# Kernel tuning notes

Hardware: AMD Instinct MI355X
Metric: run time of the kernel (lower is better)

Reference implementation:

```python
import jax, jax.numpy as jnp
import numpy as np

B, T, C = 2, 2048, 2048
N_HEAD, N_GROUPS, HEAD_SIZE = 16, 4, 128
Q_PER_KV = N_HEAD // N_GROUPS  # 4
N_ELEM = HEAD_SIZE  # rotary_percentage = 1.0
HIDDEN = 4 * C
EPS = 1e-5


def layernorm(x, w, b):
    m = jnp.mean(x, axis=-1, keepdims=True)
    v = jnp.mean(jnp.square(x - m), axis=-1, keepdims=True)
    return (x - m) * jax.lax.rsqrt(v + EPS) * w + b


def apply_rope(x, cos, sin):
    # x: [B, H, T, n_elem]; cos/sin: [T, n_elem] (broadcast over B, H)
    d = x.shape[-1]
    x1, x2 = x[..., : d // 2], x[..., d // 2 :]
    rotated = jnp.concatenate((-x2, x1), axis=-1)
    return x * cos + rotated * sin


def setup_inputs() -> dict:
    key = jax.random.key(0)
    ks = jax.random.split(key, 8)
    x = jax.random.normal(ks[0], (B, T, C), dtype=jnp.float32)
    # rope cache (NeoX/LLaMA half-rotation layout), base 10000
    theta = 1.0 / (10000.0 ** (jnp.arange(0, N_ELEM, 2, dtype=jnp.float32) / N_ELEM))
    idx_theta = jnp.outer(jnp.arange(T, dtype=jnp.float32), theta)  # [T, n_elem//2]
    idx_theta = jnp.concatenate((idx_theta, idx_theta), axis=-1)    # [T, n_elem]
    cos, sin = jnp.cos(idx_theta), jnp.sin(idx_theta)
    mask = jnp.tril(jnp.ones((T, T), dtype=bool))[None, None]  # causal [1,1,T,T]
    s = 0.02
    return {
        "x": x,
        "cos": cos,
        "sin": sin,
        "ln1_w": jnp.ones((C,), jnp.float32),
        "ln1_b": jnp.zeros((C,), jnp.float32),
        "ln2_w": jnp.ones((C,), jnp.float32),
        "ln2_b": jnp.zeros((C,), jnp.float32),
        "w_attn": jax.random.normal(ks[1], (C, (N_HEAD + 2 * N_GROUPS) * HEAD_SIZE), jnp.float32) * s,
        "w_proj": jax.random.normal(ks[2], (C, C), jnp.float32) * s,
        "w_fc": jax.random.normal(ks[3], (C, HIDDEN), jnp.float32) * s,
        "w_mlp_proj": jax.random.normal(ks[4], (HIDDEN, C), jnp.float32) * s,
        "mask": mask,
    }


def reference(x, cos, sin, ln1_w, ln1_b, ln2_w, ln2_b, w_attn, w_proj, w_fc, w_mlp_proj, mask):
    n1 = layernorm(x, ln1_w, ln1_b)
    # fused QKV projection
    qkv = n1 @ w_attn  # [B, T, (H + 2G) * hs]
    qkv = qkv.reshape(B, T, N_GROUPS, Q_PER_KV + 2, HEAD_SIZE)
    q = qkv[:, :, :, :Q_PER_KV]      # [B, T, G, qpk, hs]
    k = qkv[:, :, :, Q_PER_KV]       # [B, T, G, hs]
    v = qkv[:, :, :, Q_PER_KV + 1]   # [B, T, G, hs]
    # q -> [B, H, T, hs] (group-major head order)
    q = q.transpose(0, 2, 3, 1, 4).reshape(B, N_HEAD, T, HEAD_SIZE)
    # k, v -> [B, G, T, hs] then repeat_interleave groups to H heads
    k = jnp.repeat(k.transpose(0, 2, 1, 3), Q_PER_KV, axis=1)  # [B, H, T, hs]
    v = jnp.repeat(v.transpose(0, 2, 1, 3), Q_PER_KV, axis=1)
    # RoPE on the first N_ELEM dims (here full head)
    q = jnp.concatenate((apply_rope(q[..., :N_ELEM], cos, sin), q[..., N_ELEM:]), axis=-1)
    k = jnp.concatenate((apply_rope(k[..., :N_ELEM], cos, sin), k[..., N_ELEM:]), axis=-1)
    scale = 1.0 / np.sqrt(HEAD_SIZE).astype(np.float32)
    att = jnp.einsum("bhtd,bhsd->bhts", q, k) * scale
    att = jnp.where(mask, att, jnp.finfo(att.dtype).min)
    att = jax.nn.softmax(att, axis=-1)
    y = jnp.einsum("bhts,bhsd->bhtd", att, v)
    y = y.transpose(0, 2, 1, 3).reshape(B, T, C)
    h = y @ w_proj
    # non-parallel residual (LLaMA-style): x + attn, then x + mlp(norm2(x))
    x = x + h
    n2 = layernorm(x, ln2_w, ln2_b)
    mlp = jax.nn.gelu(n2 @ w_fc, approximate=False) @ w_mlp_proj
    return x + mlp
```

## Files before the change

### kernel.cpp

```cpp
#include <hip/hip_runtime.h>
#include <stdint.h>
#include <math.h>

#define Tn   2048
#define Cn   2048
#define BTn  4096
#define NQKV 3072
#define HID  8192

typedef unsigned short u16;
typedef float f32x4 __attribute__((ext_vector_type(4)));
typedef short s16x8 __attribute__((ext_vector_type(8)));

__device__ __forceinline__ float b2f(u16 u) { return __uint_as_float(((unsigned)u) << 16); }
__device__ __forceinline__ u16 f2b(float f) {
  unsigned i = __float_as_uint(f);
  return (u16)((i + 0x7fffu + ((i >> 16) & 1u)) >> 16);
}

__device__ __forceinline__ void g2l16(const void* g, void* l) {
  __builtin_amdgcn_global_load_lds((const __attribute__((address_space(1))) unsigned int*)g,
                                   (__attribute__((address_space(3))) unsigned int*)l,
                                   16, 0, 0);
}

__global__ __launch_bounds__(256) void transpose_f2b(const float* __restrict__ in,
                                                     u16* __restrict__ out, int R, int C) {
  __shared__ float tile[32][33];
  int bx = blockIdx.x * 32, by = blockIdx.y * 32;
  int tx = threadIdx.x, ty = threadIdx.y;
  #pragma unroll
  for (int j = 0; j < 32; j += 8)
    tile[ty + j][tx] = in[(size_t)(by + ty + j) * C + bx + tx];
  __syncthreads();
  #pragma unroll
  for (int j = 0; j < 32; j += 8)
    out[(size_t)(bx + ty + j) * R + by + tx] = f2b(tile[tx][ty + j]);
}

__global__ __launch_bounds__(256) void transpose_u16(const u16* __restrict__ in,
                                                     u16* __restrict__ out, int R, int C) {
  __shared__ u16 tile[32][33];
  const size_t zb = (size_t)blockIdx.z * R * C;
  int bx = blockIdx.x * 32, by = blockIdx.y * 32;
  int tx = threadIdx.x, ty = threadIdx.y;
  #pragma unroll
  for (int j = 0; j < 32; j += 8)
    tile[ty + j][tx] = in[zb + (size_t)(by + ty + j) * C + bx + tx];
  __syncthreads();
  #pragma unroll
  for (int j = 0; j < 32; j += 8)
    out[zb + (size_t)(bx + ty + j) * R + by + tx] = tile[tx][ty + j];
}

__global__ __launch_bounds__(256)
void copy_f32(const float* __restrict__ in, float* __restrict__ out) {
  const long i = ((long)blockIdx.x * 256 + threadIdx.x) * 4;
  *(f32x4*)(out + i) = *(const f32x4*)(in + i);
}

__global__ __launch_bounds__(256)
void layernorm_k(const float* __restrict__ x, const float* __restrict__ w,
                 const float* __restrict__ bb, u16* __restrict__ out) {
  __shared__ float red[256];
  __shared__ float sm, sv;
  const int tid = threadIdx.x;
  const long row = blockIdx.x;
  const float* xr = x + row * (long)Cn;
  float v[8];
  float s = 0.f;
  #pragma unroll
  for (int i = 0; i < 8; ++i) { v[i] = xr[i * 256 + tid]; s += v[i]; }
  red[tid] = s; __syncthreads();
  for (int st = 128; st > 0; st >>= 1) { if (tid < st) red[tid] += red[tid + st]; __syncthreads(); }
  if (tid == 0) sm = red[0] * (1.f / Cn);
  __syncthreads();
  const float mean = sm;
  float s2 = 0.f;
  #pragma unroll
  for (int i = 0; i < 8; ++i) { float d = v[i] - mean; s2 += d * d; }
  red[tid] = s2; __syncthreads();
  for (int st = 128; st > 0; st >>= 1) { if (tid < st) red[tid] += red[tid + st]; __syncthreads(); }
  if (tid == 0) sv = rsqrtf(red[0] * (1.f / Cn) + 1e-5f);
  __syncthreads();
  const float rstd = sv;
  #pragma unroll
  for (int i = 0; i < 8; ++i) {
    int c = i * 256 + tid;
    out[row * (long)Cn + c] = f2b((v[i] - mean) * rstd * w[c] + bb[c]);
  }
}

__global__ __launch_bounds__(256)
void rope_split(const u16* __restrict__ qkv, const float* __restrict__ cs,
                const float* __restrict__ sn, u16* __restrict__ q,
                u16* __restrict__ k, u16* __restrict__ v) {
  const long idx = (long)blockIdx.x * 256 + threadIdx.x;
  const int row = (int)(idx / NQKV);
  const int col = (int)(idx % NQKV);
  const int b = row >> 11, t = row & 2047;
  const int g = col / 768, rr = col % 768, s = rr >> 7, d = rr & 127;
  const u16 raw = qkv[idx];
  if (s == 5) { v[((long)(b * 4 + g) * Tn + t) * 128 + d] = raw; return; }
  const float xv = b2f(raw);
  const float x2 = b2f(qkv[idx - d + (d ^ 64)]);
  const float c = cs[t * 128 + d];
  const float si = sn[t * 128 + d];
  const float rot = (d < 64) ? -x2 : x2;
  const float o = xv * c + rot * si;
  if (s == 4) k[((long)(b * 4 + g) * Tn + t) * 128 + d] = f2b(o);
  else        q[((long)(b * 16 + g * 4 + s) * Tn + t) * 128 + d] = f2b(o);
}

__global__ __launch_bounds__(256, 2)
void attn_flash(const u16* __restrict__ q, const u16* __restrict__ k,
                const u16* __restrict__ vt, u16* __restrict__ y) {
  __shared__ __align__(16) u16 Ks[2 * 8192];
  __shared__ __align__(16) u16 Vs[2 * 8192];
  __shared__ __align__(16) u16 Ps[4][2 * 16 * 32];
  const int tid = threadIdx.x, wave = tid >> 6, lane = tid & 63;
  const int fr = lane & 15, quad = lane >> 4;
  const int lr4 = lane >> 2;
  const int su  = ((lr4 >> 3) & 1) << 1;
  const int lcs = (((lane & 3) ^ su) << 3);
  const int ksw = ((fr >> 3) & 1) << 1;
  const int rslot = (quad ^ ksw) << 3;
  const int bx = blockIdx.x, bh = blockIdx.y;
  const int b = bh >> 4, h = bh & 15, g = h >> 2;
  const int bg = b * 4 + g;
  const u16* kg = k + (size_t)bg * Tn * 128;
  const u16* vg = vt + (size_t)bg * 128 * Tn;
  const int q0 = bx * 64 + wave * 16;

  s16x8 qf[4];
  {
    const u16* qrow = q + ((size_t)bh * Tn + q0 + fr) * 128;
    #pragma unroll
    for (int kc = 0; kc < 4; ++kc)
      qf[kc] = *(const s16x8*)(qrow + kc * 32 + quad * 8);
  }
  f32x4 o_acc[8] = {};
  float m_r[4], l_r[4];
  #pragma unroll
  for (int r = 0; r < 4; ++r) { m_r[r] = -1e30f; l_r[r] = 0.f; }
  const float scale = 0.08838834764831845f;

  auto stage_kv = [&](int j0, int bufsel) {
    u16* kd = Ks + bufsel * 8192;
    u16* vd = Vs + bufsel * 8192;
    #pragma unroll
    for (int kc = 0; kc < 4; ++kc)
      g2l16(kg + (size_t)(j0 + wave * 16 + lr4) * 128 + kc * 32 + lcs,
            kd + kc * 2048 + wave * 512);
    #pragma unroll
    for (int kc = 0; kc < 2; ++kc)
      #pragma unroll
      for (int hh = 0; hh < 2; ++hh)
        g2l16(vg + (size_t)(wave * 32 + hh * 16 + lr4) * Tn + j0 + kc * 32 + lcs,
              vd + kc * 4096 + (wave * 32 + hh * 16) * 32);
  };

  stage_kv(0, 0);
  asm volatile("s_waitcnt vmcnt(0)" ::: "memory");
  __builtin_amdgcn_s_barrier();

  int cur = 0;
  for (int step = 0; step <= bx; ++step) {
    const int j0 = step * 64;
    if (step < bx) stage_kv(j0 + 64, cur ^ 1);
    const u16* kcur = Ks + cur * 8192;
    const u16* vcur = Vs + cur * 8192;

    f32x4 s[4] = {};
    __builtin_amdgcn_s_setprio(1);
    #pragma unroll
    for (int kc = 0; kc < 4; ++kc)
      #pragma unroll
      for (int nt = 0; nt < 4; ++nt) {
        s16x8 bf = *(const s16x8*)(kcur + kc * 2048 + (nt * 16 + fr) * 32 + rslot);
        s[nt] = __builtin_amdgcn_mfma_f32_16x16x32_bf16(qf[kc], bf, s[nt], 0, 0, 0);
      }
    __builtin_amdgcn_s_setprio(0);

    const bool diag = (step == bx);
    #pragma unroll
    for (int r = 0; r < 4; ++r) {
      float vmax = -1e30f;
      #pragma unroll
      for (int nt = 0; nt < 4; ++nt) {
        float sv = s[nt][r] * scale;
        if (diag && (j0 + nt * 16 + fr) > (q0 + quad * 4 + r)) sv = -1e30f;
        s[nt][r] = sv;
        vmax = fmaxf(vmax, sv);
      }
      #pragma unroll
      for (int mk = 1; mk < 16; mk <<= 1) vmax = fmaxf(vmax, __shfl_xor(vmax, mk, 64));
      const float mnew = fmaxf(m_r[r], vmax);
      const float alpha = __expf(m_r[r] - mnew);
      float rsum = 0.f;
      #pragma unroll
      for (int nt = 0; nt < 4; ++nt) {
        float pv = __expf(s[nt][r] - mnew);
        s[nt][r] = pv; rsum += pv;
      }
      #pragma unroll
      for (int mk = 1; mk < 16; mk <<= 1) rsum += __shfl_xor(rsum, mk, 64);
      l_r[r] = l_r[r] * alpha + rsum;
      m_r[r] = mnew;
      #pragma unroll
      for (int nt = 0; nt < 8; ++nt) o_acc[nt][r] *= alpha;
    }

    u16* pw = Ps[wave];
    #pragma unroll
    for (int nt = 0; nt < 4; ++nt) {
      const int col = nt * 16 + fr, pan = col >> 5, cc = col & 31;
      #pragma unroll
      for (int r = 0; r < 4; ++r) {
        const int prow = quad * 4 + r;
        pw[pan * 512 + prow * 32 + (cc ^ (((prow >> 3) & 1) << 4))] = f2b(s[nt][r]);
      }
    }
    #pragma unroll
    for (int kc = 0; kc < 2; ++kc) {
      s16x8 af = *(const s16x8*)(pw + kc * 512 + fr * 32 + rslot);
      __builtin_amdgcn_s_setprio(1);
      #pragma unroll
      for (int nt = 0; nt < 8; ++nt) {
        s16x8 bf = *(const s16x8*)(vcur + kc * 4096 + (nt * 16 + fr) * 32 + rslot);
        o_acc[nt] = __builtin_amdgcn_mfma_f32_16x16x32_bf16(af, bf, o_acc[nt], 0, 0, 0);
      }
      __builtin_amdgcn_s_setprio(0);
    }

    asm volatile("s_waitcnt vmcnt(0) lgkmcnt(0)" ::: "memory");
    __builtin_amdgcn_s_barrier();
    cur ^= 1;
  }

  #pragma unroll
  for (int r = 0; r < 4; ++r) {
    const float inv = 1.f / l_r[r];
    const size_t row = (size_t)(b * Tn + q0 + quad * 4 + r) * Cn + h * 128;
    #pragma unroll
    for (int nt = 0; nt < 8; ++nt)
      y[row + nt * 16 + fr] = f2b(o_acc[nt][r] * inv);
  }
}

#define BAR  __builtin_amdgcn_s_barrier()
#define LG0  asm volatile("s_waitcnt lgkmcnt(0)" ::: "memory")
#define RD_A(BUF, MI4)                                                                  \
  { _Pragma("unroll") for (int m_ = 0; m_ < 4; ++m_) {                                  \
      _Pragma("unroll") for (int k_ = 0; k_ < 2; ++k_)                                  \
        ar[m_][k_] = *(const s16x8*)(Sb + (BUF) * 32768 + aBase +                       \
                                     (((MI4) + m_) << 11) + (k_ << 10) + fragoff); } }
#define RD_B(BUF, NI2, DST)                                                             \
  { _Pragma("unroll") for (int n_ = 0; n_ < 2; ++n_) {                                  \
      _Pragma("unroll") for (int k_ = 0; k_ < 2; ++k_)                                  \
        DST[n_][k_] = *(const s16x8*)(Sb + (BUF) * 32768 + bBase +                      \
                                      (((NI2) + n_) << 11) + (k_ << 10) + fragoff); } }
#define MM(MB, NB, BR)                                                                  \
  { __builtin_amdgcn_s_setprio(1);                                                     \
    _Pragma("unroll") for (int m_ = 0; m_ < 4; ++m_) {                                  \
      _Pragma("unroll") for (int n_ = 0; n_ < 2; ++n_) {                                \
        _Pragma("unroll") for (int k_ = 0; k_ < 2; ++k_)                                \
          acc[(MB) + m_][(NB) + n_] = __builtin_amdgcn_mfma_f32_16x16x32_bf16(          \
              ar[m_][k_], BR[n_][k_], acc[(MB) + m_][(NB) + n_], 0, 0, 0); } }          \
    __builtin_amdgcn_s_setprio(0); }

template <int EPI>
__global__ __launch_bounds__(512, 2)
void gemm256(const u16* __restrict__ A, const u16* __restrict__ Bt,
             const float* __restrict__ res, u16* __restrict__ ob,
             float* __restrict__ of, int N, int Kl, int ld, int num_n) {
  __shared__ __align__(16) u16 S[65536];
  char* Sb = (char*)S;

  const long koff = (long)blockIdx.y * Kl;
  A += koff; Bt += koff;

  const int pid = blockIdx.x;
  const int xcd = pid & 7, idx = pid >> 3;
  const int jj = idx & 3;
  const int gp = (idx >> 2) * 8 + xcd;
  const int npc = num_n >> 1;
  const int pr = gp / npc, pc = gp - pr * npc;
  const long m0 = (long)(pr * 2 + (jj >> 1)) * 256;
  const long n0 = (long)(pc * 2 + (jj & 1)) * 256;

  const int tid = (int)threadIdx.x;
  const int wave = tid >> 6, lane = tid & 63;
  const int wr = wave >> 2, wc = wave & 3;
  const int fr = lane & 15, quad = lane >> 4;
  const int fragoff = (fr * 64 + quad * 16) ^ (((fr >> 3) & 1) << 5);
  const int aBase = wr * 16384;
  const int bBase = 65536 + (wc >> 1) * 16384 + ((wc & 1) << 13);

  int srow[2], skcb[2];
  #pragma unroll
  for (int rr = 0; rr < 2; ++rr) {
    const int d = rr * 8192 + wave * 1024 + lane * 16;
    const int l = d ^ (((d >> 9) & 1) << 5);
    srow[rr] = ((l >> 11) << 4) | ((l >> 6) & 15);
    skcb[rr] = (((l >> 10) & 1) << 6) | (l & 63);
  }
  auto stage = [&](const u16* __restrict__ src, long grow0, int kt, int regionByte) {
    #pragma unroll
    for (int rr = 0; rr < 2; ++rr)
      g2l16((const char*)src + (grow0 + srow[rr]) * (long)ld * 2 + (long)kt * 128 + skcb[rr],
            Sb + regionByte + rr * 8192 + wave * 1024);
  };

  const int nk = Kl >> 6;
  const int nk2 = nk >> 1;

  stage(A,  m0,       0, 0);
  stage(A,  m0 + 128, 0, 16384);
  stage(Bt, n0,       0, 65536);
  stage(Bt, n0 + 128, 0, 81920);
  stage(Bt, n0,       1, 98304);
  stage(Bt, n0 + 128, 1, 114688);
  asm volatile("s_waitcnt vmcnt(4)" ::: "memory");
  BAR;

  s16x8 ar[4][2], br0[2][2], br1[2][2];
  f32x4 acc[8][4] = {};

  for (int i = 0; i < nk2; ++i) {
    const int t1 = 2 * i + 1, s0 = 2 * i + 2, s1 = 2 * i + 3;
    const bool v0 = (s0 < nk), v1 = (s1 < nk);
    RD_A(0, 0); RD_B(0, 0, br0);
    stage(A, m0, t1, 32768);
    MM(0, 0, br0); LG0; BAR;
    RD_B(0, 2, br1);
    stage(A, m0 + 128, t1, 49152);
    MM(0, 2, br1); LG0; BAR;
    RD_A(0, 4);
    if (v0) stage(Bt, n0, s0, 65536);
    MM(4, 2, br1); LG0; BAR;
    if (v0) stage(Bt, n0 + 128, s0, 81920);
    MM(4, 0, br0);
    if (v0) { asm volatile("s_waitcnt vmcnt(4)" ::: "memory"); }
    else    { asm volatile("s_waitcnt vmcnt(0)" ::: "memory"); }
    BAR;
    RD_A(1, 0); RD_B(1, 0, br0);
    if (v0) stage(A, m0, s0, 0);
    MM(0, 0, br0); LG0; BAR;
    RD_B(1, 2, br1);
    if (v0) stage(A, m0 + 128, s0, 16384);
    MM(0, 2, br1); LG0; BAR;
    RD_A(1, 4);
    if (v1) stage(Bt, n0, s1, 98304);
    MM(4, 2, br1); LG0; BAR;
    if (v1) stage(Bt, n0 + 128, s1, 114688);
    MM(4, 0, br0);
    asm volatile("s_waitcnt vmcnt(4)" ::: "memory");
    BAR;
  }

  #pragma unroll
  for (int mi = 0; mi < 8; ++mi)
    #pragma unroll
    for (int ni = 0; ni < 4; ++ni)
      #pragma unroll
      for (int r = 0; r < 4; ++r) {
        const long row = m0 + wr * 128 + mi * 16 + quad * 4 + r;
        const long col = n0 + wc * 64 + ni * 16 + fr;
        const long idx2 = row * N + col;
        const float vv = acc[mi][ni][r];
        if (EPI == 0) ob[idx2] = f2b(vv);
        else if (EPI == 1) of[idx2] = vv + res[idx2];
        else if (EPI == 2) ob[idx2] = f2b(0.5f * vv * (1.0f + erff(vv * 0.70710678118654752f)));
        else atomicAdd(&of[idx2], vv);
      }
}

extern "C" void kernel_launch(void* const* d_in, const int* in_sizes, int n_in,
                              void* d_out, int out_size, void* d_ws, size_t ws_size,
                              hipStream_t stream) {
  (void)in_sizes; (void)n_in; (void)out_size; (void)ws_size;
  const float* x      = (const float*)d_in[0];
  const float* cosb   = (const float*)d_in[1];
  const float* sinb   = (const float*)d_in[2];
  const float* ln1w   = (const float*)d_in[3];
  const float* ln1b   = (const float*)d_in[4];
  const float* ln2w   = (const float*)d_in[5];
  const float* ln2b   = (const float*)d_in[6];
  const float* w_attn = (const float*)d_in[7];
  const float* w_proj = (const float*)d_in[8];
  const float* w_fc   = (const float*)d_in[9];
  const float* w_mp   = (const float*)d_in[10];
  float* out = (float*)d_out;

  char* p = (char*)d_ws;
  auto alloc = [&](size_t bytes) { char* r = p; p += (bytes + 255) & ~(size_t)255; return (void*)r; };
  u16*  wT_attn = (u16*)alloc((size_t)NQKV * Cn * 2);
  u16*  wT_proj = (u16*)alloc((size_t)Cn * Cn * 2);
  u16*  wT_fc   = (u16*)alloc((size_t)HID * Cn * 2);
  u16*  wT_mp   = (u16*)alloc((size_t)Cn * HID * 2);
  u16*  n12     = (u16*)alloc((size_t)BTn * Cn * 2);
  u16*  qkv     = (u16*)alloc((size_t)BTn * NQKV * 2);
  u16*  qb      = (u16*)alloc((size_t)2 * 16 * Tn * 128 * 2);
  u16*  kb      = (u16*)alloc((size_t)2 * 4 * Tn * 128 * 2);
  u16*  vb      = (u16*)alloc((size_t)2 * 4 * Tn * 128 * 2);
  float* x1     = (float*)alloc((size_t)BTn * Cn * 4);
  u16*  hbuf    = (u16*)alloc((size_t)BTn * HID * 2);
  u16*  vt      = n12;

  dim3 tb(32, 8);
  transpose_f2b<<<dim3(NQKV / 32, Cn / 32), tb, 0, stream>>>(w_attn, wT_attn, Cn, NQKV);
  transpose_f2b<<<dim3(Cn / 32, Cn / 32), tb, 0, stream>>>(w_proj, wT_proj, Cn, Cn);
  transpose_f2b<<<dim3(HID / 32, Cn / 32), tb, 0, stream>>>(w_fc, wT_fc, Cn, HID);
  transpose_f2b<<<dim3(Cn / 32, HID / 32), tb, 0, stream>>>(w_mp, wT_mp, HID, Cn);

  layernorm_k<<<BTn, 256, 0, stream>>>(x, ln1w, ln1b, n12);
  gemm256<0><<<(BTn / 256) * (NQKV / 256), 512, 0, stream>>>(n12, wT_attn, nullptr, qkv, nullptr, NQKV, Cn, Cn, NQKV / 256);
  rope_split<<<(int)(((long)BTn * NQKV) / 256), 256, 0, stream>>>(qkv, cosb, sinb, qb, kb, vb);
  transpose_u16<<<dim3(128 / 32, Tn / 32, 8), tb, 0, stream>>>(vb, vt, Tn, 128);
  attn_flash<<<dim3(Tn / 64, 32), 256, 0, stream>>>(qb, kb, vt, qkv );
  copy_f32<<<(int)(((long)BTn * Cn) / 1024), 256, 0, stream>>>(x, x1);
  gemm256<3><<<dim3((BTn / 256) * (Cn / 256), 2), 512, 0, stream>>>(qkv, wT_proj, nullptr, nullptr, x1, Cn, Cn / 2, Cn, Cn / 256);
  layernorm_k<<<BTn, 256, 0, stream>>>(x1, ln2w, ln2b, n12);
  gemm256<2><<<(BTn / 256) * (HID / 256), 512, 0, stream>>>(n12, wT_fc, nullptr, hbuf, nullptr, HID, Cn, Cn, HID / 256);
  copy_f32<<<(int)(((long)BTn * Cn) / 1024), 256, 0, stream>>>(x1, out);
  gemm256<3><<<dim3((BTn / 256) * (Cn / 256), 2), 512, 0, stream>>>(hbuf, wT_mp, nullptr, nullptr, out, Cn, HID / 2, HID, Cn / 256);
}
```

Measured before the change: 897.3 us.

## Replace staggered quarter-tile GEMM pipeline with simple double-buffered per-k-tile loop

Replaces the hand-scheduled ping-pong GEMM main loop with a plain double-buffered loop. The old loop split each k-tile into four MFMA phases with interleaved LDS reads, async global-to-LDS stages and barriers. The new loop loads all B fragments, issues the next tile's loads, runs the full 8x4 MFMA block while streaming A fragments, then waits on everything and hits one barrier per tile. This cuts barrier count and scheduling complexity, but it loses the fine-grained overlap, and the full vmcnt(0) wait exposes load latency at every tile.

Result: no change. 900.2 us (+0.3%).

```diff
diff --git a/kernel.cpp b/kernel.cpp
--- a/kernel.cpp
+++ b/kernel.cpp
@@ -249,25 +249,6 @@
 }
 
 #define BAR  __builtin_amdgcn_s_barrier()
-#define LG0  asm volatile("s_waitcnt lgkmcnt(0)" ::: "memory")
-#define RD_A(BUF, MI4)                                                                  \
-  { _Pragma("unroll") for (int m_ = 0; m_ < 4; ++m_) {                                  \
-      _Pragma("unroll") for (int k_ = 0; k_ < 2; ++k_)                                  \
-        ar[m_][k_] = *(const s16x8*)(Sb + (BUF) * 32768 + aBase +                       \
-                                     (((MI4) + m_) << 11) + (k_ << 10) + fragoff); } }
-#define RD_B(BUF, NI2, DST)                                                             \
-  { _Pragma("unroll") for (int n_ = 0; n_ < 2; ++n_) {                                  \
-      _Pragma("unroll") for (int k_ = 0; k_ < 2; ++k_)                                  \
-        DST[n_][k_] = *(const s16x8*)(Sb + (BUF) * 32768 + bBase +                      \
-                                      (((NI2) + n_) << 11) + (k_ << 10) + fragoff); } }
-#define MM(MB, NB, BR)                                                                  \
-  { __builtin_amdgcn_s_setprio(1);                                                     \
-    _Pragma("unroll") for (int m_ = 0; m_ < 4; ++m_) {                                  \
-      _Pragma("unroll") for (int n_ = 0; n_ < 2; ++n_) {                                \
-        _Pragma("unroll") for (int k_ = 0; k_ < 2; ++k_)                                \
-          acc[(MB) + m_][(NB) + n_] = __builtin_amdgcn_mfma_f32_16x16x32_bf16(          \
-              ar[m_][k_], BR[n_][k_], acc[(MB) + m_][(NB) + n_], 0, 0, 0); } }          \
-    __builtin_amdgcn_s_setprio(0); }
 
 template <int EPI>
 __global__ __launch_bounds__(512, 2)
@@ -313,49 +294,50 @@
   };
 
   const int nk = Kl >> 6;
-  const int nk2 = nk >> 1;
 
   stage(A,  m0,       0, 0);
   stage(A,  m0 + 128, 0, 16384);
   stage(Bt, n0,       0, 65536);
   stage(Bt, n0 + 128, 0, 81920);
-  stage(Bt, n0,       1, 98304);
-  stage(Bt, n0 + 128, 1, 114688);
-  asm volatile("s_waitcnt vmcnt(4)" ::: "memory");
+  asm volatile("s_waitcnt vmcnt(0)" ::: "memory");
   BAR;
 
-  s16x8 ar[4][2], br0[2][2], br1[2][2];
   f32x4 acc[8][4] = {};
 
-  for (int i = 0; i < nk2; ++i) {
-    const int t1 = 2 * i + 1, s0 = 2 * i + 2, s1 = 2 * i + 3;
-    const bool v0 = (s0 < nk), v1 = (s1 < nk);
-    RD_A(0, 0); RD_B(0, 0, br0);
-    stage(A, m0, t1, 32768);
-    MM(0, 0, br0); LG0; BAR;
-    RD_B(0, 2, br1);
-    stage(A, m0 + 128, t1, 49152);
-    MM(0, 2, br1); LG0; BAR;
-    RD_A(0, 4);
-    if (v0) stage(Bt, n0, s0, 65536);
-    MM(4, 2, br1); LG0; BAR;
-    if (v0) stage(Bt, n0 + 128, s0, 81920);
-    MM(4, 0, br0);
-    if (v0) { asm volatile("s_waitcnt vmcnt(4)" ::: "memory"); }
-    else    { asm volatile("s_waitcnt vmcnt(0)" ::: "memory"); }
-    BAR;
-    RD_A(1, 0); RD_B(1, 0, br0);
-    if (v0) stage(A, m0, s0, 0);
-    MM(0, 0, br0); LG0; BAR;
-    RD_B(1, 2, br1);
-    if (v0) stage(A, m0 + 128, s0, 16384);
-    MM(0, 2, br1); LG0; BAR;
-    RD_A(1, 4);
-    if (v1) stage(Bt, n0, s1, 98304);
-    MM(4, 2, br1); LG0; BAR;
-    if (v1) stage(Bt, n0 + 128, s1, 114688);
-    MM(4, 0, br0);
-    asm volatile("s_waitcnt vmcnt(4)" ::: "memory");
+  for (int t = 0; t < nk; ++t) {
+    const int bufB = (t & 1) * 32768;
+    const int obufB = 32768 - bufB;
+    const bool vn = (t + 1 < nk);
+
+    s16x8 br[4][2];
+    #pragma unroll
+    for (int n_ = 0; n_ < 4; ++n_)
+      #pragma unroll
+      for (int k_ = 0; k_ < 2; ++k_)
+        br[n_][k_] = *(const s16x8*)(Sb + bufB + bBase + (n_ << 11) + (k_ << 10) + fragoff);
+
+    if (vn) {
+      stage(A,  m0,       t + 1, obufB);
+      stage(A,  m0 + 128, t + 1, obufB + 16384);
+      stage(Bt, n0,       t + 1, 65536 + obufB);
+      stage(Bt, n0 + 128, t + 1, 65536 + obufB + 16384);
+    }
+
+    #pragma unroll
+    for (int m_ = 0; m_ < 8; ++m_) {
+      const char* arow = Sb + bufB + aBase + (m_ << 11) + fragoff;
+      s16x8 a0 = *(const s16x8*)(arow);
+      s16x8 a1 = *(const s16x8*)(arow + 1024);
+      __builtin_amdgcn_s_setprio(1);
+      #pragma unroll
+      for (int n_ = 0; n_ < 4; ++n_) {
+        acc[m_][n_] = __builtin_amdgcn_mfma_f32_16x16x32_bf16(a0, br[n_][0], acc[m_][n_], 0, 0, 0);
+        acc[m_][n_] = __builtin_amdgcn_mfma_f32_16x16x32_bf16(a1, br[n_][1], acc[m_][n_], 0, 0, 0);
+      }
+      __builtin_amdgcn_s_setprio(0);
+    }
+
+    asm volatile("s_waitcnt vmcnt(0) lgkmcnt(0)" ::: "memory");
     BAR;
   }
 
```
